# Performance work log

Hardware: AMD Instinct MI355X
Metric: run time of the kernel (lower is better)

## Reference

```python
import jax, jax.numpy as jnp
import numpy as np

B, N, L, K, C1 = 128, 300, 600, 19, 100  # batch, num_cnns, input_length, filter_size, fc hidden
PS = 7  # pool size == stride
LC = L - (K - 1)               # 582, conv output length
LP = (LC - PS) // PS + 1       # 83, pooled length
NC = 2                         # num_classes
EPS = 1e-5


def _bn(x, g, b, m, v):
    # eval-mode batchnorm, params broadcast along given axes already
    return g * (x - m) * jax.lax.rsqrt(v + EPS) + b


def setup_inputs() -> dict:
    key = jax.random.key(0)
    ks = jax.random.split(key, 20)
    f = lambda i, shape, s=0.1: (jax.random.normal(ks[i], shape, dtype=jnp.float32) * s)
    pv = lambda i, shape: (jax.random.uniform(ks[i], shape, dtype=jnp.float32) + 0.5)
    return {
        'x': jax.random.normal(ks[0], (B, 4, L), dtype=jnp.float32),
        'conv_w': f(1, (N, 4, K)), 'conv_b': f(2, (N,)),
        'bn1_g': pv(3, (N,)), 'bn1_b': f(4, (N,)), 'bn1_m': f(5, (N,)), 'bn1_v': pv(6, (N,)),
        'fc1_w': f(7, (N, C1, LP)), 'fc1_b': f(8, (N, C1)),
        'bn2_g': pv(9, (N, C1)), 'bn2_b': f(10, (N, C1)), 'bn2_m': f(11, (N, C1)), 'bn2_v': pv(12, (N, C1)),
        'fc2_w': f(13, (N, C1)), 'fc2_b': f(14, (N,)),
        'bn3_g': pv(15, (N,)), 'bn3_b': f(16, (N,)), 'bn3_m': f(17, (N,)), 'bn3_v': pv(18, (N,)),
        'final_w': f(19, (NC, N)), 'final_b': jnp.zeros((NC,), dtype=jnp.float32),
    }


def reference(x, conv_w, conv_b, bn1_g, bn1_b, bn1_m, bn1_v,
              fc1_w, fc1_b, bn2_g, bn2_b, bn2_m, bn2_v,
              fc2_w, fc2_b, bn3_g, bn3_b, bn3_m, bn3_v,
              final_w, final_b):
    # grouped conv on a repeated input == plain conv with 4 in-channels, N out-channels
    h = jax.lax.conv_general_dilated(x, conv_w, window_strides=(1,), padding='VALID',
                                     dimension_numbers=('NCH', 'OIH', 'NCH'))  # [B,N,582]
    h = h + conv_b[None, :, None]
    h = _bn(h, bn1_g[None, :, None], bn1_b[None, :, None], bn1_m[None, :, None], bn1_v[None, :, None])
    h = jnp.exp(h)
    # MaxPool1d(7,7): [B,N,582] -> [B,N,83]
    h = jax.lax.reduce_window(h, -jnp.inf, jax.lax.max,
                              window_dimensions=(1, 1, PS), window_strides=(1, 1, PS), padding='VALID')
    # grouped 1x1 conv == per-unit dense: [B,N,83] x [N,100,83] -> [B,N,100]
    h = jnp.einsum('bnp,nhp->bnh', h, fc1_w) + fc1_b[None]
    h = jax.nn.relu(_bn(h, bn2_g[None], bn2_b[None], bn2_m[None], bn2_v[None]))
    # second grouped 1x1 conv: [B,N,100] x [N,100] -> [B,N]
    h = jnp.einsum('bnh,nh->bn', h, fc2_w) + fc2_b[None]
    h = jax.nn.relu(_bn(h, bn3_g[None], bn3_b[None], bn3_m[None], bn3_v[None]))
    return h @ final_w.T + final_b  # [B,num_classes]
```

## Files before the change

kernel.cpp:

```cpp
#include <hip/hip_runtime.h>
#include <math.h>

#define EPS_ 1e-5f

__global__ __launch_bounds__(256) void kP(const float* __restrict__ conv_w,
                                          float* __restrict__ cw4) {
    const int cq = blockIdx.x;
    const int c  = cq / 5;
    const int kq = cq - c * 5;
    for (int n = threadIdx.x; n < 300; n += 256) {
        float4 v;
        const int k0 = 4 * kq;
        v.x = (k0 + 0 < 19) ? conv_w[n * 76 + c * 19 + k0 + 0] : 0.f;
        v.y = (k0 + 1 < 19) ? conv_w[n * 76 + c * 19 + k0 + 1] : 0.f;
        v.z = (k0 + 2 < 19) ? conv_w[n * 76 + c * 19 + k0 + 2] : 0.f;
        v.w = (k0 + 3 < 19) ? conv_w[n * 76 + c * 19 + k0 + 3] : 0.f;
        reinterpret_cast<float4*>(cw4)[(c * 5 + kq) * 300 + n] = v;
    }
}

__global__ __launch_bounds__(128) void kA(
        const float* __restrict__ x,
        const float* __restrict__ cw4,
        const float* __restrict__ conv_b,
        const float* __restrict__ g1, const float* __restrict__ b1,
        const float* __restrict__ m1, const float* __restrict__ v1,
        float* __restrict__ pooled)
{
    const int id  = blockIdx.x;
    const int b   = id / 56;
    const int i2  = id - b * 56;
    const int wv  = __builtin_amdgcn_readfirstlane(threadIdx.x >> 6);
    const int sub = i2 * 2 + wv;
    if (sub >= 105) return;
    const int ng  = sub / 21;
    const int pc  = sub - ng * 21;
    const int p0c = pc * 4;
    const int p0  = (p0c > 79) ? 79 : p0c;
    const int lane = threadIdx.x & 63;
    const int n   = ng * 64 + lane;
    const int nc  = (n < 300) ? n : 299;

    const float4* w4 = reinterpret_cast<const float4*>(cw4);

    float acc[28];
    #pragma unroll
    for (int i = 0; i < 28; ++i) acc[i] = 0.f;

    #pragma unroll 1
    for (int c = 0; c < 4; ++c) {
        const float* xc = x + b * 2400 + c * 600 + 7 * p0;
        float xw[46];
        #pragma unroll
        for (int j = 0; j < 46; ++j) xw[j] = xc[j];
        #pragma unroll
        for (int kq = 0; kq < 5; ++kq) {
            const float4 wv4 = w4[(c * 5 + kq) * 300 + nc];
            const int ni = (kq == 4) ? 3 : 4;
            #pragma unroll
            for (int i = 0; i < ni; ++i) {
                const int k = 4 * kq + i;
                const float wvv = (i == 0) ? wv4.x : (i == 1) ? wv4.y
                                : (i == 2) ? wv4.z : wv4.w;
                #pragma unroll
                for (int p = 0; p < 4; ++p)
                    #pragma unroll
                    for (int q = 0; q < 7; ++q)
                        acc[p * 7 + q] = fmaf(xw[7 * p + q + k], wvv,
                                              acc[p * 7 + q]);
            }
        }
    }

    const float A1 = g1[nc] * rsqrtf(v1[nc] + EPS_);
    const float B1 = fmaf(A1, conv_b[nc] - m1[nc], b1[nc]);
    if (n < 300) {
        float* op = pooled + ((size_t)n * 83 + p0) * 128 + b;
        #pragma unroll
        for (int p = 0; p < 4; ++p) {
            float mx = -INFINITY;
            #pragma unroll
            for (int q = 0; q < 7; ++q)
                mx = fmaxf(mx, fmaf(A1, acc[p * 7 + q], B1));
            op[p * 128] = __expf(mx);
        }
    }
}

__global__ __launch_bounds__(256) void kB(
        const float* __restrict__ pooled,
        const float* __restrict__ fc1w,
        const float* __restrict__ fc1b,
        const float* __restrict__ g2, const float* __restrict__ b2,
        const float* __restrict__ m2, const float* __restrict__ v2,
        const float* __restrict__ fc2w,
        float* __restrict__ sp)
{
    __shared__ float sW[83 * 60];
    __shared__ float sRed[4][64];
    const int id  = blockIdx.x;
    const int n   = id >> 2;
    const int rem = id & 3;
    const int bh  = rem >> 1;
    const int hq  = rem & 1;
    const int tid = threadIdx.x;

    {
        const float* src = fc1w + (size_t)n * 8300 + hq * 50 * 83;
        for (int i = tid; i < 4150; i += 256) {
            const int h = i / 83, p = i - h * 83;
            sW[p * 60 + h] = src[i];
        }
        for (int i = tid; i < 830; i += 256) {
            const int p = i / 10, h = 50 + (i - p * 10);
            sW[p * 60 + h] = 0.f;
        }
    }
    __syncthreads();

    const int lane = tid & 63;
    const int wv   = __builtin_amdgcn_readfirstlane(tid >> 6);
    const int h0   = wv * 13;
    const int nh   = (wv < 3) ? 13 : 11;
    const int bb   = bh * 64 + lane;

    const float* pp = pooled + (size_t)n * 83 * 128 + bb;

    float acc[13];
    #pragma unroll
    for (int j = 0; j < 13; ++j) acc[j] = 0.f;

    #pragma unroll 4
    for (int p = 0; p < 83; ++p) {
        const float pv = pp[p * 128];
        const float* wrow = sW + p * 60 + h0;
        #pragma unroll
        for (int j = 0; j < 13; ++j)
            acc[j] = fmaf(wrow[j], pv, acc[j]);
    }

    const int hbase = n * 100 + hq * 50 + h0;
    float part = 0.f;
    for (int j = 0; j < nh; ++j) {
        const int hi = hbase + j;
        const float A2 = g2[hi] * rsqrtf(v2[hi] + EPS_);
        const float C2 = fmaf(A2, fc1b[hi] - m2[hi], b2[hi]);
        part = fmaf(fmaxf(fmaf(A2, acc[j], C2), 0.f), fc2w[hi], part);
    }
    sRed[wv][lane] = part;
    __syncthreads();

    if (tid < 64) {
        const float s = sRed[0][tid] + sRed[1][tid] + sRed[2][tid] + sRed[3][tid];
        sp[((size_t)hq * 300 + n) * 128 + bh * 64 + tid] = s;
    }
}

__global__ __launch_bounds__(64) void kC(
        const float* __restrict__ sp,
        const float* __restrict__ fc2b,
        const float* __restrict__ g3, const float* __restrict__ b3,
        const float* __restrict__ m3, const float* __restrict__ v3,
        const float* __restrict__ fw,
        const float* __restrict__ fb,
        float* __restrict__ out)
{
    const int b = blockIdx.x, t = threadIdx.x;
    float a0 = 0.f, a1 = 0.f;
    for (int nn = t; nn < 300; nn += 64) {
        const float s = sp[nn * 128 + b] + sp[(300 + nn) * 128 + b] + fc2b[nn];
        const float A3 = g3[nn] * rsqrtf(v3[nn] + EPS_);
        const float z = fmaxf(fmaf(A3, s - m3[nn], b3[nn]), 0.f);
        a0 = fmaf(z, fw[nn], a0);
        a1 = fmaf(z, fw[300 + nn], a1);
    }
    #pragma unroll
    for (int off = 32; off > 0; off >>= 1) {
        a0 += __shfl_xor(a0, off, 64);
        a1 += __shfl_xor(a1, off, 64);
    }
    if (t == 0) {
        out[b * 2 + 0] = a0 + fb[0];
        out[b * 2 + 1] = a1 + fb[1];
    }
}

extern "C" void kernel_launch(void* const* d_in, const int* in_sizes, int n_in,
                              void* d_out, int out_size, void* d_ws, size_t ws_size,
                              hipStream_t stream) {
    const float* x      = (const float*)d_in[0];
    const float* conv_w = (const float*)d_in[1];
    const float* conv_b = (const float*)d_in[2];
    const float* g1 = (const float*)d_in[3];
    const float* b1 = (const float*)d_in[4];
    const float* m1 = (const float*)d_in[5];
    const float* v1 = (const float*)d_in[6];
    const float* fc1_w = (const float*)d_in[7];
    const float* fc1_b = (const float*)d_in[8];
    const float* g2 = (const float*)d_in[9];
    const float* b2 = (const float*)d_in[10];
    const float* m2 = (const float*)d_in[11];
    const float* v2 = (const float*)d_in[12];
    const float* fc2_w = (const float*)d_in[13];
    const float* fc2_b = (const float*)d_in[14];
    const float* g3 = (const float*)d_in[15];
    const float* b3 = (const float*)d_in[16];
    const float* m3 = (const float*)d_in[17];
    const float* v3 = (const float*)d_in[18];
    const float* fw = (const float*)d_in[19];
    const float* fb = (const float*)d_in[20];
    float* out = (float*)d_out;

    float* pooled = (float*)d_ws;
    float* sp     = pooled + (size_t)300 * 83 * 128;
    float* cw4    = sp + 76800;

    kP<<<20, 256, 0, stream>>>(conv_w, cw4);
    kA<<<128 * 56, 128, 0, stream>>>(x, cw4, conv_b, g1, b1, m1, v1, pooled);
    kB<<<1200, 256, 0, stream>>>(pooled, fc1_w, fc1_b, g2, b2, m2, v2,
                                 fc2_w, sp);
    kC<<<128, 64, 0, stream>>>(sp, fc2_b, g3, b3, m3, v3, fw, fb, out);
}
```

Measured before the change: 173.8 us.

## Stage input row in shared memory and loop conv tiles per wave in kA

The conv kernel now launches 512 blocks of 448 threads, four blocks per batch row. Each block copies that row's 2400-float input into shared memory once, and each wave loops over four (channel-group, pool-chunk) tiles instead of one. This removes the repeated global reads of x done by the old 7168 small blocks and cuts block launch overhead. In exchange, the grid is much smaller, per-wave work is serialized, and duplicate tiles at the clamped tail are recomputed and rewritten. Occupancy also drops because of register pressure under the larger block size.

```diff
diff --git a/kernel.cpp b/kernel.cpp
--- a/kernel.cpp
+++ b/kernel.cpp
@@ -19,7 +19,7 @@
     }
 }
 
-__global__ __launch_bounds__(128) void kA(
+__global__ __launch_bounds__(448) void kA(
         const float* __restrict__ x,
         const float* __restrict__ cw4,
         const float* __restrict__ conv_b,
@@ -27,62 +27,77 @@
         const float* __restrict__ m1, const float* __restrict__ v1,
         float* __restrict__ pooled)
 {
-    const int id  = blockIdx.x;
-    const int b   = id / 56;
-    const int i2  = id - b * 56;
-    const int wv  = __builtin_amdgcn_readfirstlane(threadIdx.x >> 6);
-    const int sub = i2 * 2 + wv;
-    if (sub >= 105) return;
-    const int ng  = sub / 21;
-    const int pc  = sub - ng * 21;
-    const int p0c = pc * 4;
-    const int p0  = (p0c > 79) ? 79 : p0c;
-    const int lane = threadIdx.x & 63;
-    const int n   = ng * 64 + lane;
-    const int nc  = (n < 300) ? n : 299;
-
+    const int bq = blockIdx.x;
+    const int b  = bq >> 2;
+    const int qt = bq & 3;
+    const int tid = threadIdx.x;
+
+    __shared__ float sX[2400];
+
+    {
+        const float4* xsrc = reinterpret_cast<const float4*>(x + b * 2400);
+        float4* sX4 = reinterpret_cast<float4*>(sX);
+        for (int i = tid; i < 600; i += 448) sX4[i] = xsrc[i];
+    }
+    __syncthreads();
+
+    const int w    = __builtin_amdgcn_readfirstlane(tid >> 6);
+    const int lane = tid & 63;
     const float4* w4 = reinterpret_cast<const float4*>(cw4);
 
-    float acc[28];
-    #pragma unroll
-    for (int i = 0; i < 28; ++i) acc[i] = 0.f;
-
     #pragma unroll 1
-    for (int c = 0; c < 4; ++c) {
-        const float* xc = x + b * 2400 + c * 600 + 7 * p0;
-        float xw[46];
+    for (int t = 0; t < 4; ++t) {
+        const int tau = qt + 4 * (7 * t + w);
+        const int tc  = (tau > 104) ? 104 : tau;
+        const int ng  = tc / 21;
+        const int pc  = tc - ng * 21;
+        const int p0c = pc * 4;
+        const int p0  = (p0c > 79) ? 79 : p0c;
+        const int n   = ng * 64 + lane;
+        const int nc  = (n < 300) ? n : 299;
+
+        float acc[28];
         #pragma unroll
-        for (int j = 0; j < 46; ++j) xw[j] = xc[j];
-        #pragma unroll
-        for (int kq = 0; kq < 5; ++kq) {
-            const float4 wv4 = w4[(c * 5 + kq) * 300 + nc];
-            const int ni = (kq == 4) ? 3 : 4;
+        for (int i = 0; i < 28; ++i) acc[i] = 0.f;
+
+        #pragma unroll 1
+        for (int c = 0; c < 4; ++c) {
+            const float* xc = sX + c * 600 + 7 * p0;
+            float xw[46];
             #pragma unroll
-            for (int i = 0; i < ni; ++i) {
-                const int k = 4 * kq + i;
-                const float wvv = (i == 0) ? wv4.x : (i == 1) ? wv4.y
-                                : (i == 2) ? wv4.z : wv4.w;
+            for (int j = 0; j < 46; ++j) xw[j] = xc[j];
+
+            #pragma unroll
+            for (int kq = 0; kq < 5; ++kq) {
+                const float4 wv4 = w4[(c * 5 + kq) * 300 + nc];
+                const int ni = (kq == 4) ? 3 : 4;
                 #pragma unroll
-                for (int p = 0; p < 4; ++p)
+                for (int i = 0; i < ni; ++i) {
+                    const int k = 4 * kq + i;
+                    const float wvv = (i == 0) ? wv4.x : (i == 1) ? wv4.y
+                                    : (i == 2) ? wv4.z : wv4.w;
                     #pragma unroll
-                    for (int q = 0; q < 7; ++q)
-                        acc[p * 7 + q] = fmaf(xw[7 * p + q + k], wvv,
-                                              acc[p * 7 + q]);
+                    for (int p = 0; p < 4; ++p)
+                        #pragma unroll
+                        for (int q = 0; q < 7; ++q)
+                            acc[p * 7 + q] = fmaf(xw[7 * p + q + k], wvv,
+                                                  acc[p * 7 + q]);
+                }
             }
         }
-    }
-
-    const float A1 = g1[nc] * rsqrtf(v1[nc] + EPS_);
-    const float B1 = fmaf(A1, conv_b[nc] - m1[nc], b1[nc]);
-    if (n < 300) {
-        float* op = pooled + ((size_t)n * 83 + p0) * 128 + b;
-        #pragma unroll
-        for (int p = 0; p < 4; ++p) {
-            float mx = -INFINITY;
+
+        const float A1 = g1[nc] * rsqrtf(v1[nc] + EPS_);
+        const float B1 = fmaf(A1, conv_b[nc] - m1[nc], b1[nc]);
+        if (n < 300) {
+            float* op = pooled + ((size_t)n * 83 + p0) * 128 + b;
             #pragma unroll
-            for (int q = 0; q < 7; ++q)
-                mx = fmaxf(mx, fmaf(A1, acc[p * 7 + q], B1));
-            op[p * 128] = __expf(mx);
+            for (int p = 0; p < 4; ++p) {
+                float mx = -INFINITY;
+                #pragma unroll
+                for (int q = 0; q < 7; ++q)
+                    mx = fmaxf(mx, fmaf(A1, acc[p * 7 + q], B1));
+                op[p * 128] = __expf(mx);
+            }
         }
     }
 }
@@ -216,7 +231,7 @@
     float* cw4    = sp + 76800;
 
     kP<<<20, 256, 0, stream>>>(conv_w, cw4);
-    kA<<<128 * 56, 128, 0, stream>>>(x, cw4, conv_b, g1, b1, m1, v1, pooled);
+    kA<<<512, 448, 0, stream>>>(x, cw4, conv_b, g1, b1, m1, v1, pooled);
     kB<<<1200, 256, 0, stream>>>(pooled, fc1_w, fc1_b, g2, b2, m2, v2,
                                  fc2_w, sp);
     kC<<<128, 64, 0, stream>>>(sp, fc2_b, g3, b3, m3, v3, fw, fb, out);
```

Result: slower. 190.9 us (+9.8%).

## Fuse final classifier into FC kernel via atomics and preload conv weights

Applied to the files above, without the earlier changes.

Removes the last kernel by having each FC block compute a whole unit's 100 hidden outputs, apply BN3/ReLU, and atomically add its contribution to the two output logits; the bias init moves into the prep kernel. The FC block now stages the full 83x100 weight slice in shared memory (padded stride 101) and each wave keeps 25 accumulators, halving the grid. The conv kernel loads all 20 weight float4s into registers up front and fully unrolls the channel loop. This saves a launch and the partial-sum round trip, at the cost of register pressure, more shared memory per block, and nondeterministic float atomic ordering.

```diff
diff --git a/kernel.cpp b/kernel.cpp
--- a/kernel.cpp
+++ b/kernel.cpp
@@ -4,10 +4,13 @@
 #define EPS_ 1e-5f
 
 __global__ __launch_bounds__(256) void kP(const float* __restrict__ conv_w,
-                                          float* __restrict__ cw4) {
+                                          float* __restrict__ cw4,
+                                          const float* __restrict__ fb,
+                                          float* __restrict__ out) {
     const int cq = blockIdx.x;
     const int c  = cq / 5;
     const int kq = cq - c * 5;
+    if (cq == 0) out[threadIdx.x] = fb[threadIdx.x & 1];
     for (int n = threadIdx.x; n < 300; n += 256) {
         float4 v;
         const int k0 = 4 * kq;
@@ -43,11 +46,15 @@
 
     const float4* w4 = reinterpret_cast<const float4*>(cw4);
 
+    float4 wreg[20];
+    #pragma unroll
+    for (int cq = 0; cq < 20; ++cq) wreg[cq] = w4[cq * 300 + nc];
+
     float acc[28];
     #pragma unroll
     for (int i = 0; i < 28; ++i) acc[i] = 0.f;
 
-    #pragma unroll 1
+    #pragma unroll
     for (int c = 0; c < 4; ++c) {
         const float* xc = x + b * 2400 + c * 600 + 7 * p0;
         float xw[46];
@@ -55,7 +62,7 @@
         for (int j = 0; j < 46; ++j) xw[j] = xc[j];
         #pragma unroll
         for (int kq = 0; kq < 5; ++kq) {
-            const float4 wv4 = w4[(c * 5 + kq) * 300 + nc];
+            const float4 wv4 = wreg[c * 5 + kq];
             const int ni = (kq == 4) ? 3 : 4;
             #pragma unroll
             for (int i = 0; i < ni; ++i) {
@@ -94,54 +101,52 @@
         const float* __restrict__ g2, const float* __restrict__ b2,
         const float* __restrict__ m2, const float* __restrict__ v2,
         const float* __restrict__ fc2w,
-        float* __restrict__ sp)
+        const float* __restrict__ fc2b,
+        const float* __restrict__ g3, const float* __restrict__ b3,
+        const float* __restrict__ m3, const float* __restrict__ v3,
+        const float* __restrict__ fw,
+        float* __restrict__ out)
 {
-    __shared__ float sW[83 * 60];
+    __shared__ float sW[83 * 101];
     __shared__ float sRed[4][64];
     const int id  = blockIdx.x;
-    const int n   = id >> 2;
-    const int rem = id & 3;
-    const int bh  = rem >> 1;
-    const int hq  = rem & 1;
+    const int n   = id >> 1;
+    const int bh  = id & 1;
     const int tid = threadIdx.x;
 
     {
-        const float* src = fc1w + (size_t)n * 8300 + hq * 50 * 83;
-        for (int i = tid; i < 4150; i += 256) {
+        const float* src = fc1w + (size_t)n * 8300;
+        for (int i = tid; i < 8300; i += 256) {
             const int h = i / 83, p = i - h * 83;
-            sW[p * 60 + h] = src[i];
-        }
-        for (int i = tid; i < 830; i += 256) {
-            const int p = i / 10, h = 50 + (i - p * 10);
-            sW[p * 60 + h] = 0.f;
+            sW[p * 101 + h] = src[i];
         }
     }
     __syncthreads();
 
     const int lane = tid & 63;
     const int wv   = __builtin_amdgcn_readfirstlane(tid >> 6);
-    const int h0   = wv * 13;
-    const int nh   = (wv < 3) ? 13 : 11;
+    const int h0   = wv * 25;
     const int bb   = bh * 64 + lane;
 
     const float* pp = pooled + (size_t)n * 83 * 128 + bb;
 
-    float acc[13];
-    #pragma unroll
-    for (int j = 0; j < 13; ++j) acc[j] = 0.f;
-
-    #pragma unroll 4
+    float acc[25];
+    #pragma unroll
+    for (int j = 0; j < 25; ++j) acc[j] = 0.f;
+
+    #pragma unroll 8
     for (int p = 0; p < 83; ++p) {
         const float pv = pp[p * 128];
-        const float* wrow = sW + p * 60 + h0;
-        #pragma unroll
-        for (int j = 0; j < 13; ++j)
+        const float* wrow = sW + p * 101 + h0;
+        #pragma unroll
+        for (int j = 0; j < 25; ++j)
             acc[j] = fmaf(wrow[j], pv, acc[j]);
     }
 
-    const int hbase = n * 100 + hq * 50 + h0;
+    const int hbase = n * 100 + h0;
     float part = 0.f;
-    for (int j = 0; j < nh; ++j) {
+    #pragma unroll 5
+    for (int j = 0; j < 25; ++j) {
         const int hi = hbase + j;
         const float A2 = g2[hi] * rsqrtf(v2[hi] + EPS_);
         const float C2 = fmaf(A2, fc1b[hi] - m2[hi], b2[hi]);
@@ -151,37 +156,13 @@
     __syncthreads();
 
     if (tid < 64) {
-        const float s = sRed[0][tid] + sRed[1][tid] + sRed[2][tid] + sRed[3][tid];
-        sp[((size_t)hq * 300 + n) * 128 + bh * 64 + tid] = s;
-    }
-}
-
-__global__ __launch_bounds__(64) void kC(
-        const float* __restrict__ sp,
-        const float* __restrict__ fc2b,
-        const float* __restrict__ g3, const float* __restrict__ b3,
-        const float* __restrict__ m3, const float* __restrict__ v3,
-        const float* __restrict__ fw,
-        const float* __restrict__ fb,
-        float* __restrict__ out)
-{
-    const int b = blockIdx.x, t = threadIdx.x;
-    float a0 = 0.f, a1 = 0.f;
-    for (int nn = t; nn < 300; nn += 64) {
-        const float s = sp[nn * 128 + b] + sp[(300 + nn) * 128 + b] + fc2b[nn];
-        const float A3 = g3[nn] * rsqrtf(v3[nn] + EPS_);
-        const float z = fmaxf(fmaf(A3, s - m3[nn], b3[nn]), 0.f);
-        a0 = fmaf(z, fw[nn], a0);
-        a1 = fmaf(z, fw[300 + nn], a1);
-    }
-    #pragma unroll
-    for (int off = 32; off > 0; off >>= 1) {
-        a0 += __shfl_xor(a0, off, 64);
-        a1 += __shfl_xor(a1, off, 64);
-    }
-    if (t == 0) {
-        out[b * 2 + 0] = a0 + fb[0];
-        out[b * 2 + 1] = a1 + fb[1];
+        const float s = sRed[0][tid] + sRed[1][tid] + sRed[2][tid]
+                      + sRed[3][tid] + fc2b[n];
+        const float A3 = g3[n] * rsqrtf(v3[n] + EPS_);
+        const float z  = fmaxf(fmaf(A3, s - m3[n], b3[n]), 0.f);
+        const int bi   = bh * 64 + tid;
+        atomicAdd(&out[bi * 2 + 0], z * fw[n]);
+        atomicAdd(&out[bi * 2 + 1], z * fw[300 + n]);
     }
 }
 
@@ -212,12 +193,10 @@
     float* out = (float*)d_out;
 
     float* pooled = (float*)d_ws;
-    float* sp     = pooled + (size_t)300 * 83 * 128;
-    float* cw4    = sp + 76800;
-
-    kP<<<20, 256, 0, stream>>>(conv_w, cw4);
+    float* cw4    = pooled + (size_t)300 * 83 * 128;
+
+    kP<<<20, 256, 0, stream>>>(conv_w, cw4, fb, out);
     kA<<<128 * 56, 128, 0, stream>>>(x, cw4, conv_b, g1, b1, m1, v1, pooled);
-    kB<<<1200, 256, 0, stream>>>(pooled, fc1_w, fc1_b, g2, b2, m2, v2,
-                                 fc2_w, sp);
-    kC<<<128, 64, 0, stream>>>(sp, fc2_b, g3, b3, m3, v3, fw, fb, out);
-}
+    kB<<<600, 256, 0, stream>>>(pooled, fc1_w, fc1_b, g2, b2, m2, v2,
+                                fc2_w, fc2_b, g3, b3, m3, v3, fw, out);
+}
```

Result: slower. 197.6 us (+13.7%).
